# Kernel tuning notes

Hardware: AMD Instinct MI355X
Metric: run time of the kernel (lower is better)

The kernel has to match this reference:

```python
import jax, jax.numpy as jnp
import numpy as np
import math

B, S, H, NH, D = 2, 2048, 4096, 32, 128
MAX_POS = 4096


def _make_rope_table(num_pos, dim):
    # create_sinusoidal_positions: cat(sin, cos) each of width dim//2
    inv_freq = 1.0 / (10000.0 ** (np.arange(0, dim, 2, dtype=np.float32) / dim))
    t = np.arange(num_pos, dtype=np.float32)
    ang = np.einsum('i,j->ij', t, inv_freq)  # [num_pos, dim//2]
    return jnp.asarray(np.concatenate([np.sin(ang), np.cos(ang)], axis=1), dtype=jnp.float32)


def setup_inputs() -> dict:
    key = jax.random.key(0)
    ks = jax.random.split(key, 5)
    hidden_states = jax.random.normal(ks[0], (B, S, H), dtype=jnp.float32)
    position_ids = jnp.broadcast_to(jnp.arange(S, dtype=jnp.int32), (B, S))
    # additive causal mask: 0 on/below diagonal, large negative above
    neg = jnp.finfo(jnp.float32).min
    causal = jnp.where(jnp.tril(jnp.ones((S, S), dtype=bool)), 0.0, neg)
    attention_mask = jnp.broadcast_to(causal[None, None], (B, 1, S, S)).astype(jnp.float32)
    scale = 1.0 / math.sqrt(H)
    Wq = jax.random.normal(ks[1], (H, H), dtype=jnp.float32) * scale
    Wk = jax.random.normal(ks[2], (H, H), dtype=jnp.float32) * scale
    Wv = jax.random.normal(ks[3], (H, H), dtype=jnp.float32) * scale
    Wo = jax.random.normal(ks[4], (H, H), dtype=jnp.float32) * scale
    rope_table = _make_rope_table(MAX_POS, D)
    return {"hidden_states": hidden_states, "position_ids": position_ids,
            "attention_mask": attention_mask, "Wq": Wq, "Wk": Wk, "Wv": Wv,
            "Wo": Wo, "rope_table": rope_table}


def _apply_rope(x, sin, cos):
    # x: [b, s, nh, d]; sin/cos: [b, s, 1, d//2] (llama half-split rotate)
    x1, x2 = x[..., : D // 2], x[..., D // 2:]
    return jnp.concatenate([x1 * cos - x2 * sin, x2 * cos + x1 * sin], axis=-1)


def reference(hidden_states, position_ids, attention_mask, Wq, Wk, Wv, Wo, rope_table):
    b, s, _ = hidden_states.shape
    q = jnp.einsum('bsh,oh->bso', hidden_states, Wq).reshape(b, s, NH, D)
    k = jnp.einsum('bsh,oh->bso', hidden_states, Wk).reshape(b, s, NH, D)
    v = jnp.einsum('bsh,oh->bso', hidden_states, Wv).reshape(b, s, NH, D)

    emb = rope_table[position_ids]                       # [b, s, d]
    sin = emb[..., : D // 2][:, :, None, :]              # [b, s, 1, d//2]
    cos = emb[..., D // 2:][:, :, None, :]
    q = _apply_rope(q, sin, cos)
    k = _apply_rope(k, sin, cos)

    # [b, nh, q, k]
    scores = jnp.einsum('bqhd,bkhd->bhqk', q, k) / math.sqrt(D)
    scores = scores + attention_mask
    scores = jnp.maximum(scores, jnp.finfo(scores.dtype).min)
    probs = jax.nn.softmax(scores.astype(jnp.float32), axis=-1).astype(q.dtype)
    attn = jnp.einsum('bhqk,bkhd->bqhd', probs, v).reshape(b, s, H)
    return jnp.einsum('bso,ho->bsh', attn, Wo)
```

## Files before the change

kernel.cpp:

```cpp
#include <hip/hip_runtime.h>
#include <math.h>

#define B_  2
#define S_  2048
#define H_  4096
#define NH_ 32
#define D_  128
#define M_  (B_*S_)

typedef __attribute__((ext_vector_type(8))) __bf16 bf16x8;
typedef __attribute__((ext_vector_type(8))) unsigned short ushort8v;
typedef __attribute__((ext_vector_type(4))) float floatx4;
typedef __attribute__((ext_vector_type(2))) unsigned int uint2v;

__device__ inline unsigned short f2bf(float f) {
  unsigned u = __float_as_uint(f);
  u += 0x7FFF + ((u >> 16) & 1);
  return (unsigned short)(u >> 16);
}
__device__ inline float bf2f(unsigned short s) {
  return __uint_as_float(((unsigned)s) << 16);
}

__global__ __launch_bounds__(256)
void cast_f32_bf16(const float* __restrict__ s, unsigned short* __restrict__ d) {
  int i = (blockIdx.x * 256 + threadIdx.x) * 8;
  float4 a = *(const float4*)(s + i);
  float4 b = *(const float4*)(s + i + 4);
  ushort8v o;
  o[0] = f2bf(a.x); o[1] = f2bf(a.y); o[2] = f2bf(a.z); o[3] = f2bf(a.w);
  o[4] = f2bf(b.x); o[5] = f2bf(b.y); o[6] = f2bf(b.z); o[7] = f2bf(b.w);
  *(ushort8v*)(d + i) = o;
}

#define TT 128
#define TK 32

__device__ inline void cstore(float* p, float v) { *p = v; }
__device__ inline void cstore(unsigned short* p, float v) { *p = f2bf(v); }

template <typename OT>
__global__ __launch_bounds__(256)
void gemm_bt_mfma(const unsigned short* __restrict__ A,
                  const unsigned short* __restrict__ Bt,
                  OT* __restrict__ C, int M, int N, int K) {
  __shared__ unsigned short As[TT * TK];
  __shared__ unsigned short Bs[TT * TK];
  const int t  = threadIdx.x;
  const int w  = t >> 6;
  const int l  = t & 63;
  const int wm = (w & 1) * 64;
  const int wn = (w >> 1) * 64;
  const int m0 = blockIdx.y * TT;
  const int n0 = blockIdx.x * TT;

  const int srow = l >> 2;
  const int scol = (l & 3) * 8;
  const unsigned short* agp = A  + (size_t)(m0 + w * 32 + srow) * K + scol;
  const unsigned short* bgp = Bt + (size_t)(n0 + w * 32 + srow) * K + scol;
  unsigned short* asd = As + w * 1024;
  unsigned short* bsd = Bs + w * 1024;

  floatx4 acc[4][4] = {};
  const int lr = l & 15;
  const int kq = (l >> 4) * 8;

  for (int k0 = 0; k0 < K; k0 += TK) {
    __syncthreads();
    __builtin_amdgcn_global_load_lds(
        (const __attribute__((address_space(1))) void*)(agp + k0),
        (__attribute__((address_space(3))) void*)(asd), 16, 0, 0);
    __builtin_amdgcn_global_load_lds(
        (const __attribute__((address_space(1))) void*)(agp + (size_t)16 * K + k0),
        (__attribute__((address_space(3))) void*)(asd + 512), 16, 0, 0);
    __builtin_amdgcn_global_load_lds(
        (const __attribute__((address_space(1))) void*)(bgp + k0),
        (__attribute__((address_space(3))) void*)(bsd), 16, 0, 0);
    __builtin_amdgcn_global_load_lds(
        (const __attribute__((address_space(1))) void*)(bgp + (size_t)16 * K + k0),
        (__attribute__((address_space(3))) void*)(bsd + 512), 16, 0, 0);
    __syncthreads();

    bf16x8 af[4], bfr[4];
#pragma unroll
    for (int i = 0; i < 4; ++i) {
      af[i]  = *(const bf16x8*)(As + (wm + i * 16 + lr) * TK + kq);
      bfr[i] = *(const bf16x8*)(Bs + (wn + i * 16 + lr) * TK + kq);
    }
#pragma unroll
    for (int mi = 0; mi < 4; ++mi)
#pragma unroll
      for (int ni = 0; ni < 4; ++ni)
        acc[mi][ni] = __builtin_amdgcn_mfma_f32_16x16x32_bf16(
            af[mi], bfr[ni], acc[mi][ni], 0, 0, 0);
  }

  const int rg = (l >> 4) * 4;
#pragma unroll
  for (int mi = 0; mi < 4; ++mi)
#pragma unroll
    for (int ni = 0; ni < 4; ++ni)
#pragma unroll
      for (int i = 0; i < 4; ++i) {
        size_t row = (size_t)m0 + wm + mi * 16 + rg + i;
        size_t col = (size_t)n0 + wn + ni * 16 + lr;
        cstore(&C[row * N + col], acc[mi][ni][i]);
      }
}

__global__ __launch_bounds__(256)
void rope_qk(unsigned short* __restrict__ q, unsigned short* __restrict__ k,
             const int* __restrict__ pos, const float* __restrict__ rt) {
  int idx = blockIdx.x * 256 + threadIdx.x;
  int d  = idx & 63;
  int h  = (idx >> 6) & (NH_ - 1);
  int bs = idx >> 11;
  int p  = pos[bs];
  float sv = rt[p * D_ + d];
  float cv = rt[p * D_ + 64 + d];
  size_t base = ((size_t)bs * NH_ + h) * D_;
  float x1 = bf2f(q[base + d]), x2 = bf2f(q[base + 64 + d]);
  q[base + d]      = f2bf(x1 * cv - x2 * sv);
  q[base + 64 + d] = f2bf(x2 * cv + x1 * sv);
  x1 = bf2f(k[base + d]); x2 = bf2f(k[base + 64 + d]);
  k[base + d]      = f2bf(x1 * cv - x2 * sv);
  k[base + 64 + d] = f2bf(x2 * cv + x1 * sv);
}

#define QB 128
#define KB 64

__global__ __launch_bounds__(256)
void flash_fwd_mfma(const unsigned short* __restrict__ qg,
                    const unsigned short* __restrict__ kg,
                    const unsigned short* __restrict__ vg,
                    unsigned short* __restrict__ ob) {
  __shared__ unsigned short Ks[KB * 128];
  __shared__ unsigned short Vt[128 * KB];
  __shared__ unsigned short Ps[4 * 32 * KB];

  const int q0 = blockIdx.x * QB;
  const int h  = blockIdx.y;
  const int b  = blockIdx.z;
  const int t  = threadIdx.x;
  const int w  = t >> 6;
  const int l  = t & 63;
  const int g  = l >> 4;
  const int m  = l & 15;
  const int qmin = q0 + w * 32;
  const float scale = 0.088388347648318447f;

  bf16x8 qf[2][4];
#pragma unroll
  for (int qt = 0; qt < 2; ++qt)
#pragma unroll
    for (int dc = 0; dc < 4; ++dc)
      qf[qt][dc] = *(const bf16x8*)&qg[((size_t)(b * S_ + qmin + qt * 16 + m) * NH_ + h) * D_
                                       + dc * 32 + g * 8];

  floatx4 o_acc[2][8] = {};
  float m_run[2] = {-3.0e38f, -3.0e38f};
  float l_run[2] = {0.f, 0.f};

  unsigned short* PsW = Ps + w * (32 * KB);
  const int gx = g ^ (m & 7);
  const int vx = gx ^ (m >> 3);

  for (int k0 = 0; k0 < q0 + QB; k0 += KB) {
    __syncthreads();
#pragma unroll
    for (int j = 0; j < 4; ++j) {
      int r = w * 16 + j * 4 + g;
      int c = m ^ (r & 7);
      const unsigned short* src =
          kg + ((size_t)(b * S_ + k0 + r) * NH_ + h) * D_ + c * 8;
      __builtin_amdgcn_global_load_lds(
          (const __attribute__((address_space(1))) void*)src,
          (__attribute__((address_space(3))) void*)(Ks + (w * 16 + j * 4) * 128),
          16, 0, 0);
    }
#pragma unroll
    for (int it = 0; it < 4; ++it) {
      int r = w * 4 + it * 16 + g;
      ushort8v vr = *(const ushort8v*)&vg[((size_t)(b * S_ + k0 + r) * NH_ + h) * D_ + m * 8];
      int bi = 512 * m + (r & 7);
      int bx = (r >> 3) ^ (m & 7);
#pragma unroll
      for (int j = 0; j < 8; ++j)
        Vt[bi + j * 64 + ((bx ^ j) << 3)] = vr[j];
    }
    __syncthreads();

    if (k0 <= qmin + 31) {
      floatx4 sacc[4][2] = {};
#pragma unroll
      for (int kt = 0; kt < 4; ++kt) {
        const unsigned short* krow = Ks + (kt * 16 + m) * 128;
#pragma unroll
        for (int dc = 0; dc < 4; ++dc) {
          bf16x8 kf = *(const bf16x8*)&krow[(gx ^ (dc << 2)) << 3];
          sacc[kt][0] = __builtin_amdgcn_mfma_f32_16x16x32_bf16(kf, qf[0][dc], sacc[kt][0], 0, 0, 0);
          sacc[kt][1] = __builtin_amdgcn_mfma_f32_16x16x32_bf16(kf, qf[1][dc], sacc[kt][1], 0, 0, 0);
        }
      }

      const bool diag = (k0 + KB - 1 > qmin);
#pragma unroll
      for (int qt = 0; qt < 2; ++qt) {
        const int qglob = qmin + qt * 16 + m;
        float p[16];
#pragma unroll
        for (int kt = 0; kt < 4; ++kt)
#pragma unroll
          for (int i = 0; i < 4; ++i) {
            float v = sacc[kt][qt][i];
            if (diag && (k0 + kt * 16 + 4 * g + i > qglob)) v = -1e30f;
            p[kt * 4 + i] = v;
          }
        float tm = p[0];
#pragma unroll
        for (int j = 1; j < 16; ++j) tm = fmaxf(tm, p[j]);
        tm = fmaxf(tm, __shfl_xor(tm, 16));
        tm = fmaxf(tm, __shfl_xor(tm, 32));
        if (__any(tm > m_run[qt] + 64.f)) {
          float mn = fmaxf(m_run[qt], tm);
          float al = __expf((m_run[qt] - mn) * scale);
          m_run[qt] = mn;
          l_run[qt] *= al;
#pragma unroll
          for (int i = 0; i < 4; ++i) {
            float ao = __shfl(al, g * 20 + i);
#pragma unroll
            for (int dt = 0; dt < 8; ++dt) o_acc[qt][dt][i] *= ao;
          }
        }
        const float ms = m_run[qt];
        float psum = 0.f;
#pragma unroll
        for (int j = 0; j < 16; ++j) {
          p[j] = __expf((p[j] - ms) * scale);
          psum += p[j];
        }
        psum += __shfl_xor(psum, 16);
        psum += __shfl_xor(psum, 32);
        l_run[qt] += psum;
        unsigned short* pr = PsW + (qt * 16 + m) * KB;
#pragma unroll
        for (int kt = 0; kt < 4; ++kt) {
          uint2v pk;
          pk[0] = (unsigned)f2bf(p[kt * 4 + 0]) | ((unsigned)f2bf(p[kt * 4 + 1]) << 16);
          pk[1] = (unsigned)f2bf(p[kt * 4 + 2]) | ((unsigned)f2bf(p[kt * 4 + 3]) << 16);
          int slot = (kt << 1) ^ (g >> 1) ^ (m & 7);
          *(uint2v*)&pr[slot * 8 + (g & 1) * 4] = pk;
        }
      }

#pragma unroll
      for (int kc = 0; kc < 2; ++kc) {
        bf16x8 pa0 = *(const bf16x8*)&PsW[m * KB + ((gx ^ (kc << 2)) << 3)];
        bf16x8 pa1 = *(const bf16x8*)&PsW[(16 + m) * KB + ((gx ^ (kc << 2)) << 3)];
#pragma unroll
        for (int dt = 0; dt < 8; ++dt) {
          bf16x8 vt = *(const bf16x8*)&Vt[(dt * 16 + m) * KB
                                          + ((vx ^ (kc << 2) ^ ((2 * dt) & 7)) << 3)];
          o_acc[0][dt] = __builtin_amdgcn_mfma_f32_16x16x32_bf16(pa0, vt, o_acc[0][dt], 0, 0, 0);
          o_acc[1][dt] = __builtin_amdgcn_mfma_f32_16x16x32_bf16(pa1, vt, o_acc[1][dt], 0, 0, 0);
        }
      }
    }
  }

#pragma unroll
  for (int qt = 0; qt < 2; ++qt) {
    float inv = 1.f / l_run[qt];
#pragma unroll
    for (int i = 0; i < 4; ++i) {
      float iv = __shfl(inv, g * 20 + i);
      size_t base = ((size_t)(b * S_ + qmin + qt * 16 + 4 * g + i) * NH_ + h) * D_ + m;
#pragma unroll
      for (int dt = 0; dt < 8; ++dt)
        ob[base + dt * 16] = f2bf(o_acc[qt][dt][i] * iv);
    }
  }
}

extern "C" void kernel_launch(void* const* d_in, const int* in_sizes, int n_in,
                              void* d_out, int out_size, void* d_ws, size_t ws_size,
                              hipStream_t stream) {
  const float* X   = (const float*)d_in[0];
  const int*   pid = (const int*)d_in[1];
  const float* Wq  = (const float*)d_in[3];
  const float* Wk  = (const float*)d_in[4];
  const float* Wv  = (const float*)d_in[5];
  const float* Wo  = (const float*)d_in[6];
  const float* rt  = (const float*)d_in[7];
  float* out = (float*)d_out;

  const size_t NE = (size_t)M_ * H_;
  unsigned short* Xb  = (unsigned short*)d_ws;
  unsigned short* Wqb = Xb  + NE;
  unsigned short* Wkb = Wqb + NE;
  unsigned short* Wvb = Wkb + NE;
  unsigned short* Wob = Wvb + NE;
  unsigned short* qb  = Wob + NE;
  unsigned short* kb  = qb  + NE;
  unsigned short* vb  = kb  + NE;
  unsigned short* ab  = Xb;

  dim3 bk(256);
  int cblocks = (int)(NE / 2048);
  cast_f32_bf16<<<cblocks, bk, 0, stream>>>(X,  Xb);
  cast_f32_bf16<<<cblocks, bk, 0, stream>>>(Wq, Wqb);
  cast_f32_bf16<<<cblocks, bk, 0, stream>>>(Wk, Wkb);
  cast_f32_bf16<<<cblocks, bk, 0, stream>>>(Wv, Wvb);
  cast_f32_bf16<<<cblocks, bk, 0, stream>>>(Wo, Wob);

  dim3 gg(H_ / TT, M_ / TT);
  gemm_bt_mfma<unsigned short><<<gg, bk, 0, stream>>>(Xb, Wqb, qb, M_, H_, H_);
  gemm_bt_mfma<unsigned short><<<gg, bk, 0, stream>>>(Xb, Wkb, kb, M_, H_, H_);
  gemm_bt_mfma<unsigned short><<<gg, bk, 0, stream>>>(Xb, Wvb, vb, M_, H_, H_);

  rope_qk<<<dim3((M_ * NH_ * 64) / 256), bk, 0, stream>>>(qb, kb, pid, rt);

  flash_fwd_mfma<<<dim3(S_ / QB, NH_, B_), bk, 0, stream>>>(qb, kb, vb, ab);

  gemm_bt_mfma<float><<<gg, bk, 0, stream>>>(ab, Wob, out, M_, H_, H_);
}
```

Measured before the change: 1.664 ms.

## Double-buffer K/V loads, reorder blocks longest-first, pass P via permlane swaps

The flash attention kernel now double-buffers K in LDS and prefetches the next V tile into registers while the current tile computes, then writes V transposed with packed 4-element stores. The grid is flattened and ordered so the longest causal query blocks are scheduled first for better load balance. The P matrix no longer round-trips through LDS; it is rearranged into the MFMA operand layout with v_permlane32/16_swap instructions. This adds LDS usage and register pressure, and the permlane layout mapping must match the old LDS layout exactly.

```diff
diff --git a/kernel.cpp b/kernel.cpp
--- a/kernel.cpp
+++ b/kernel.cpp
@@ -10,8 +10,8 @@
 
 typedef __attribute__((ext_vector_type(8))) __bf16 bf16x8;
 typedef __attribute__((ext_vector_type(8))) unsigned short ushort8v;
+typedef __attribute__((ext_vector_type(4))) unsigned short ushort4v;
 typedef __attribute__((ext_vector_type(4))) float floatx4;
-typedef __attribute__((ext_vector_type(2))) unsigned int uint2v;
 
 __device__ inline unsigned short f2bf(float f) {
   unsigned u = __float_as_uint(f);
@@ -135,13 +135,16 @@
                     const unsigned short* __restrict__ kg,
                     const unsigned short* __restrict__ vg,
                     unsigned short* __restrict__ ob) {
-  __shared__ unsigned short Ks[KB * 128];
+  __shared__ unsigned short Ks[2 * KB * 128];
   __shared__ unsigned short Vt[128 * KB];
-  __shared__ unsigned short Ps[4 * 32 * KB];
-
-  const int q0 = blockIdx.x * QB;
-  const int h  = blockIdx.y;
-  const int b  = blockIdx.z;
+
+  const int bid = blockIdx.x;
+  const int qb  = (S_ / QB) - 1 - (bid >> 6);
+  const int hb  = bid & 63;
+  const int h   = hb >> 1;
+  const int b   = hb & 1;
+  const int q0  = qb * QB;
+
   const int t  = threadIdx.x;
   const int w  = t >> 6;
   const int l  = t & 63;
@@ -149,6 +152,7 @@
   const int m  = l & 15;
   const int qmin = q0 + w * 32;
   const float scale = 0.088388347648318447f;
+  const int nt = (q0 + QB) / KB;
 
   bf16x8 qf[2][4];
 #pragma unroll
@@ -162,40 +166,63 @@
   float m_run[2] = {-3.0e38f, -3.0e38f};
   float l_run[2] = {0.f, 0.f};
 
-  unsigned short* PsW = Ps + w * (32 * KB);
   const int gx = g ^ (m & 7);
   const int vx = gx ^ (m >> 3);
-
-  for (int k0 = 0; k0 < q0 + QB; k0 += KB) {
-    __syncthreads();
-#pragma unroll
-    for (int j = 0; j < 4; ++j) {
-      int r = w * 16 + j * 4 + g;
-      int c = m ^ (r & 7);
-      const unsigned short* src =
-          kg + ((size_t)(b * S_ + k0 + r) * NH_ + h) * D_ + c * 8;
-      __builtin_amdgcn_global_load_lds(
-          (const __attribute__((address_space(1))) void*)src,
-          (__attribute__((address_space(3))) void*)(Ks + (w * 16 + j * 4) * 128),
-          16, 0, 0);
-    }
-#pragma unroll
-    for (int it = 0; it < 4; ++it) {
-      int r = w * 4 + it * 16 + g;
-      ushort8v vr = *(const ushort8v*)&vg[((size_t)(b * S_ + k0 + r) * NH_ + h) * D_ + m * 8];
-      int bi = 512 * m + (r & 7);
-      int bx = (r >> 3) ^ (m & 7);
-#pragma unroll
-      for (int j = 0; j < 8; ++j)
-        Vt[bi + j * 64 + ((bx ^ j) << 3)] = vr[j];
-    }
-    __syncthreads();
+  const int cV  = 2 * w + (g >> 1);
+  const int icV = 4 * (g & 1);
+
+  ushort8v vreg[4];
+
+#pragma unroll
+  for (int j = 0; j < 4; ++j) {
+    int r = w * 16 + j * 4 + g;
+    int c = m ^ (r & 7);
+    const unsigned short* src = kg + ((size_t)(b * S_ + r) * NH_ + h) * D_ + c * 8;
+    __builtin_amdgcn_global_load_lds(
+        (const __attribute__((address_space(1))) void*)src,
+        (__attribute__((address_space(3))) void*)(Ks + (w * 16 + j * 4) * 128), 16, 0, 0);
+  }
+#pragma unroll
+  for (int j = 0; j < 4; ++j)
+    vreg[j] = *(const ushort8v*)&vg[((size_t)(b * S_ + w * 16 + 4 * g + j) * NH_ + h) * D_ + m * 8];
+  __syncthreads();
+#pragma unroll
+  for (int e = 0; e < 8; ++e) {
+    int d = m * 8 + e;
+    int slot = cV ^ ((d & 7) ^ ((d >> 3) & 7));
+    ushort4v pk;
+    pk[0] = vreg[0][e]; pk[1] = vreg[1][e]; pk[2] = vreg[2][e]; pk[3] = vreg[3][e];
+    *(ushort4v*)&Vt[d * 64 + slot * 8 + icV] = pk;
+  }
+  __syncthreads();
+
+  for (int ti = 0; ti < nt; ++ti) {
+    const int k0 = ti * KB;
+    const unsigned short* KsC = Ks + (ti & 1) * (KB * 128);
+    unsigned short* KsN = Ks + ((ti + 1) & 1) * (KB * 128);
+    const bool more = (ti + 1 < nt);
+
+    if (more) {
+      const int k1 = k0 + KB;
+#pragma unroll
+      for (int j = 0; j < 4; ++j) {
+        int r = w * 16 + j * 4 + g;
+        int c = m ^ (r & 7);
+        const unsigned short* src = kg + ((size_t)(b * S_ + k1 + r) * NH_ + h) * D_ + c * 8;
+        __builtin_amdgcn_global_load_lds(
+            (const __attribute__((address_space(1))) void*)src,
+            (__attribute__((address_space(3))) void*)(KsN + (w * 16 + j * 4) * 128), 16, 0, 0);
+      }
+#pragma unroll
+      for (int j = 0; j < 4; ++j)
+        vreg[j] = *(const ushort8v*)&vg[((size_t)(b * S_ + k1 + w * 16 + 4 * g + j) * NH_ + h) * D_ + m * 8];
+    }
 
     if (k0 <= qmin + 31) {
       floatx4 sacc[4][2] = {};
 #pragma unroll
       for (int kt = 0; kt < 4; ++kt) {
-        const unsigned short* krow = Ks + (kt * 16 + m) * 128;
+        const unsigned short* krow = KsC + (kt * 16 + m) * 128;
 #pragma unroll
         for (int dc = 0; dc < 4; ++dc) {
           bf16x8 kf = *(const bf16x8*)&krow[(gx ^ (dc << 2)) << 3];
@@ -205,6 +232,7 @@
       }
 
       const bool diag = (k0 + KB - 1 > qmin);
+      unsigned plo[2][4], phi[2][4];
 #pragma unroll
       for (int qt = 0; qt < 2; ++qt) {
         const int qglob = qmin + qt * 16 + m;
@@ -244,30 +272,48 @@
         psum += __shfl_xor(psum, 16);
         psum += __shfl_xor(psum, 32);
         l_run[qt] += psum;
-        unsigned short* pr = PsW + (qt * 16 + m) * KB;
 #pragma unroll
         for (int kt = 0; kt < 4; ++kt) {
-          uint2v pk;
-          pk[0] = (unsigned)f2bf(p[kt * 4 + 0]) | ((unsigned)f2bf(p[kt * 4 + 1]) << 16);
-          pk[1] = (unsigned)f2bf(p[kt * 4 + 2]) | ((unsigned)f2bf(p[kt * 4 + 3]) << 16);
-          int slot = (kt << 1) ^ (g >> 1) ^ (m & 7);
-          *(uint2v*)&pr[slot * 8 + (g & 1) * 4] = pk;
+          plo[qt][kt] = (unsigned)f2bf(p[kt * 4 + 0]) | ((unsigned)f2bf(p[kt * 4 + 1]) << 16);
+          phi[qt][kt] = (unsigned)f2bf(p[kt * 4 + 2]) | ((unsigned)f2bf(p[kt * 4 + 3]) << 16);
         }
       }
 
 #pragma unroll
       for (int kc = 0; kc < 2; ++kc) {
-        bf16x8 pa0 = *(const bf16x8*)&PsW[m * KB + ((gx ^ (kc << 2)) << 3)];
-        bf16x8 pa1 = *(const bf16x8*)&PsW[(16 + m) * KB + ((gx ^ (kc << 2)) << 3)];
+        union { unsigned u[4]; bf16x8 v; } pu[2];
+#pragma unroll
+        for (int qt = 0; qt < 2; ++qt) {
+          unsigned a0 = plo[qt][2 * kc], b0 = plo[qt][2 * kc + 1];
+          asm("v_permlane32_swap_b32 %0, %1" : "+v"(a0), "+v"(b0));
+          asm("v_permlane16_swap_b32 %0, %1" : "+v"(a0), "+v"(b0));
+          unsigned a1 = phi[qt][2 * kc], b1 = phi[qt][2 * kc + 1];
+          asm("v_permlane32_swap_b32 %0, %1" : "+v"(a1), "+v"(b1));
+          asm("v_permlane16_swap_b32 %0, %1" : "+v"(a1), "+v"(b1));
+          pu[qt].u[0] = a0; pu[qt].u[1] = a1; pu[qt].u[2] = b0; pu[qt].u[3] = b1;
+        }
 #pragma unroll
         for (int dt = 0; dt < 8; ++dt) {
-          bf16x8 vt = *(const bf16x8*)&Vt[(dt * 16 + m) * KB
+          bf16x8 vt = *(const bf16x8*)&Vt[(dt * 16 + m) * 64
                                           + ((vx ^ (kc << 2) ^ ((2 * dt) & 7)) << 3)];
-          o_acc[0][dt] = __builtin_amdgcn_mfma_f32_16x16x32_bf16(pa0, vt, o_acc[0][dt], 0, 0, 0);
-          o_acc[1][dt] = __builtin_amdgcn_mfma_f32_16x16x32_bf16(pa1, vt, o_acc[1][dt], 0, 0, 0);
-        }
-      }
-    }
+          o_acc[0][dt] = __builtin_amdgcn_mfma_f32_16x16x32_bf16(pu[0].v, vt, o_acc[0][dt], 0, 0, 0);
+          o_acc[1][dt] = __builtin_amdgcn_mfma_f32_16x16x32_bf16(pu[1].v, vt, o_acc[1][dt], 0, 0, 0);
+        }
+      }
+    }
+
+    __syncthreads();
+    if (more) {
+#pragma unroll
+      for (int e = 0; e < 8; ++e) {
+        int d = m * 8 + e;
+        int slot = cV ^ ((d & 7) ^ ((d >> 3) & 7));
+        ushort4v pk;
+        pk[0] = vreg[0][e]; pk[1] = vreg[1][e]; pk[2] = vreg[2][e]; pk[3] = vreg[3][e];
+        *(ushort4v*)&Vt[d * 64 + slot * 8 + icV] = pk;
+      }
+    }
+    __syncthreads();
   }
 
 #pragma unroll
@@ -322,7 +368,7 @@
 
   rope_qk<<<dim3((M_ * NH_ * 64) / 256), bk, 0, stream>>>(qb, kb, pid, rt);
 
-  flash_fwd_mfma<<<dim3(S_ / QB, NH_, B_), bk, 0, stream>>>(qb, kb, vb, ab);
+  flash_fwd_mfma<<<dim3((S_ / QB) * NH_ * B_), bk, 0, stream>>>(qb, kb, vb, ab);
 
   gemm_bt_mfma<float><<<gg, bk, 0, stream>>>(ab, Wob, out, M_, H_, H_);
 }
```

New measurement: 1.355 ms. 1.23x faster.
